# Optimization experiments

Measured on AMD Instinct MI355X. Metric: run time of the kernel, lower is better.

The kernel has to match this reference:

```python
import jax, jax.numpy as jnp
import numpy as np
import math

B, S, D, H = 4, 1024, 1024, 16
DK = D // H
NEG = -1e32


def _split_heads(x):
    # [B,S,D] -> [B,H,S,DK]
    return x.reshape(B, S, H, DK).transpose(0, 2, 1, 3)


def _merge_heads(x):
    # [B,H,S,DK] -> [B,S,D]
    return x.transpose(0, 2, 1, 3).reshape(B, S, D)


def _lin(x, w, b):
    # torch nn.Linear: y = x @ W^T + b, W is [out,in]
    return x @ w.T + b


def _decay_attn(scores, mask_f, gamma_val, pos):
    # scores: [B,H,S,S]; mask_f float {0,1}; gamma_val [1,H,1,1]; pos [S,S]
    def dist_fn(sc):
        p = jax.nn.softmax(jnp.where(mask_f == 0, NEG, sc), axis=-1) * mask_f
        cum = jnp.cumsum(p, axis=-1)
        tot = jnp.sum(p, axis=-1, keepdims=True)
        return jnp.sqrt(jnp.clip((tot - cum) * pos, 0.0))
    dist = jax.lax.stop_gradient(dist_fn(scores))  # torch.no_grad + detach
    eff = jnp.clip(jnp.exp(dist * gamma_val), 1e-5, 1e5)
    s = jnp.where(mask_f == 0, NEG, scores * eff)
    return jax.nn.softmax(s, axis=-1)


def _forward(mask, qmean, qcov, kmean, kcov, vmean, vcov,
             wq_m, bq_m, wq_c, bq_c, wk_m, bk_m, wk_c, bk_c,
             wv_m, bv_m, wv_c, bv_c, wo_m, bo_m, wo_c, bo_c, gammas):
    qm = _split_heads(_lin(qmean, wq_m, bq_m))
    qc = _split_heads(_lin(qcov, wq_c, bq_c))
    km = _split_heads(_lin(kmean, wk_m, bk_m))
    kc = _split_heads(_lin(kcov, wk_c, bk_c))
    vm = _split_heads(_lin(vmean, wv_m, bv_m))
    vc = _split_heads(_lin(vcov, wv_c, bv_c))

    scale = 1.0 / math.sqrt(DK)
    scores_mean = jnp.einsum('bhqd,bhkd->bhqk', qm, km) * scale
    scores_cov = jnp.einsum('bhqd,bhkd->bhqk', qc, kc) * scale

    mask_f = mask.astype(jnp.float32)
    idx = jnp.arange(S, dtype=jnp.float32)
    pos = jnp.abs(idx[None, :] - idx[:, None])  # |i-j| [S,S]
    gamma_val = -jax.nn.softplus(gammas)[None]  # [1,H,1,1]

    pm = _decay_attn(scores_mean, mask_f, gamma_val, pos)
    pc = _decay_attn(scores_cov, mask_f, gamma_val, pos)
    om = jnp.einsum('bhqk,bhkd->bhqd', pm, vm)
    oc = jnp.einsum('bhqk,bhkd->bhqd', pc, vc)

    out_mean = _lin(_merge_heads(om), wo_m, bo_m)
    out_cov = _lin(_merge_heads(oc), wo_c, bo_c)
    return out_mean, out_cov


def setup_inputs() -> dict:
    key = jax.random.key(0)
    ks = jax.random.split(key, 24)
    inp = {}
    tnames = ['query_mean', 'query_cov', 'key_mean', 'key_cov', 'values_mean', 'values_cov']
    for i, n in enumerate(tnames):
        inp[n] = jax.random.normal(ks[i], (B, S, D), jnp.float32)
    inp['mask'] = jnp.tril(jnp.ones((S, S), jnp.int32))[None, None]  # causal
    wnames = ['wq_m', 'wq_c', 'wk_m', 'wk_c', 'wv_m', 'wv_c', 'wo_m', 'wo_c']
    bound = math.sqrt(6.0 / (D + D))  # xavier_uniform
    for i, n in enumerate(wnames):
        inp[n] = jax.random.uniform(ks[6 + i], (D, D), jnp.float32, -bound, bound)
        inp['b' + n[1:]] = jnp.zeros((D,), jnp.float32)
    inp['gammas'] = jax.random.uniform(ks[20], (H, 1, 1), jnp.float32, -1.0, 1.0)
    return inp


def reference(query_mean, query_cov, key_mean, key_cov, values_mean, values_cov, mask,
              wq_m, bq_m, wq_c, bq_c, wk_m, bk_m, wk_c, bk_c,
              wv_m, bv_m, wv_c, bv_c, wo_m, bo_m, wo_c, bo_c, gammas):
    return _forward(mask, query_mean, query_cov, key_mean, key_cov, values_mean, values_cov,
                    wq_m, bq_m, wq_c, bq_c, wk_m, bk_m, wk_c, bk_c,
                    wv_m, bv_m, wv_c, bv_c, wo_m, bo_m, wo_c, bo_c, gammas)
```

## Files before the change

### kernel.cpp

```cpp
#include <hip/hip_runtime.h>
#include <math.h>

#define NTOK 4096
typedef unsigned int uint;

__device__ __forceinline__ int split_idx(int n, int d) {
  int b = n >> 10, s = n & 1023, h = d >> 6, dk = d & 63;
  return (((b << 4) + h) << 16) + (s << 6) + dk;
}

__device__ __forceinline__ ushort bf16_rne(float f) {
  uint u = __float_as_uint(f);
  return (ushort)((u + 0x7FFFu + ((u >> 16) & 1u)) >> 16);
}
__device__ __forceinline__ float bf16f(ushort h) {
  return __uint_as_float(((uint)h) << 16);
}

typedef __attribute__((ext_vector_type(8))) short bf16x8;
typedef __attribute__((ext_vector_type(4))) float f32x4;

__device__ __forceinline__ void gload16(const void* g, void* l) {
  __builtin_amdgcn_global_load_lds(
      (const __attribute__((address_space(1))) void*)g,
      (__attribute__((address_space(3))) void*)l, 16, 0, 0);
}

struct ConvP {
  const float4* s[14];
  ushort* hi[14];
  ushort* lo[14];
  int n4[14];
};
__global__ __launch_bounds__(256) void convert_split(ConvP C) {
  const int z = blockIdx.z;
  const int id = blockIdx.x * 256 + threadIdx.x;
  if (id >= C.n4[z]) return;
  const float4 x = C.s[z][id];
  const float xs[4] = {x.x, x.y, x.z, x.w};
  ushort hs[4], ls[4];
#pragma unroll
  for (int k = 0; k < 4; ++k) {
    hs[k] = bf16_rne(xs[k]);
    ls[k] = bf16_rne(xs[k] - bf16f(hs[k]));
  }
  ushort4 hv; hv.x = hs[0]; hv.y = hs[1]; hv.z = hs[2]; hv.w = hs[3];
  ushort4 lv; lv.x = ls[0]; lv.y = ls[1]; lv.z = ls[2]; lv.w = ls[3];
  *(ushort4*)&C.hi[z][id * 4] = hv;
  *(ushort4*)&C.lo[z][id * 4] = lv;
}

struct MG {
  const char* ah[6]; const char* al[6];
  const char* bh[6]; const char* bl[6];
  const float* bias[6]; float* y[6];
};

template<bool SPLIT_IN, bool SPLIT_OUT>
__global__ __launch_bounds__(256, 3) void gemm_mfma(MG P) {
  __shared__ ushort sAhi[4096], sAlo[4096], sBhi[4096], sBlo[4096];
  const int z = blockIdx.z;
  const char* __restrict__ Ah = P.ah[z];
  const char* __restrict__ Al = P.al[z];
  const char* __restrict__ Bh = P.bh[z];
  const char* __restrict__ Bl = P.bl[z];

  const int t = threadIdx.x, l = t & 63, w = t >> 6;
  const int wm = w >> 1, wn = w & 1;
  const int bn0 = blockIdx.x * 128, bm0 = blockIdx.y * 128;

  int offA[2], offB[2];
  {
    const int srow = w * 16 + (l >> 2), scd = l & 3;
#pragma unroll
    for (int q = 0; q < 2; ++q) {
      const int r = srow + q * 64;
      const int cc = scd ^ ((r >> 1) & 3);
      const int m = bm0 + r, n = bn0 + r;
      offA[q] = SPLIT_IN
                    ? ((((m >> 10) << 20) + ((m & 1023) << 6) + cc * 8) * 2)
                    : (m * 2048 + cc * 16);
      offB[q] = n * 2048 + cc * 16;
    }
  }
  int aoff[4], boff[4];
  {
    const int frow = l & 15, fc = l >> 4;
#pragma unroll
    for (int f = 0; f < 4; ++f) {
      const int ra = wm * 64 + f * 16 + frow;
      aoff[f] = ra * 64 + ((fc ^ ((ra >> 1) & 3)) * 16);
      const int rb = wn * 64 + f * 16 + frow;
      boff[f] = rb * 64 + ((fc ^ ((rb >> 1) & 3)) * 16);
    }
  }

  f32x4 acc[4][4];
#pragma unroll
  for (int i = 0; i < 4; ++i)
#pragma unroll
    for (int j = 0; j < 4; ++j) acc[i][j] = (f32x4){0.f, 0.f, 0.f, 0.f};

  for (int k0 = 0; k0 < 1024; k0 += 32) {
    __syncthreads();
    const int scA = SPLIT_IN ? ((((k0 >> 6) << 16) + (k0 & 63)) * 2) : (k0 * 2);
    const int scB = k0 * 2;
    gload16(Ah + offA[0] + scA, (char*)sAhi + w * 1024);
    gload16(Ah + offA[1] + scA, (char*)sAhi + 4096 + w * 1024);
    gload16(Al + offA[0] + scA, (char*)sAlo + w * 1024);
    gload16(Al + offA[1] + scA, (char*)sAlo + 4096 + w * 1024);
    gload16(Bh + offB[0] + scB, (char*)sBhi + w * 1024);
    gload16(Bh + offB[1] + scB, (char*)sBhi + 4096 + w * 1024);
    gload16(Bl + offB[0] + scB, (char*)sBlo + w * 1024);
    gload16(Bl + offB[1] + scB, (char*)sBlo + 4096 + w * 1024);
    __syncthreads();

    bf16x8 fah[4], fal[4], fbh[4], fbl[4];
#pragma unroll
    for (int f = 0; f < 4; ++f) {
      fah[f] = *(const bf16x8*)((const char*)sAhi + aoff[f]);
      fal[f] = *(const bf16x8*)((const char*)sAlo + aoff[f]);
      fbh[f] = *(const bf16x8*)((const char*)sBhi + boff[f]);
      fbl[f] = *(const bf16x8*)((const char*)sBlo + boff[f]);
    }
#pragma unroll
    for (int fi = 0; fi < 4; ++fi)
#pragma unroll
      for (int fj = 0; fj < 4; ++fj) {
        acc[fi][fj] = __builtin_amdgcn_mfma_f32_16x16x32_bf16(
            fah[fi], fbh[fj], acc[fi][fj], 0, 0, 0);
        acc[fi][fj] = __builtin_amdgcn_mfma_f32_16x16x32_bf16(
            fah[fi], fbl[fj], acc[fi][fj], 0, 0, 0);
        acc[fi][fj] = __builtin_amdgcn_mfma_f32_16x16x32_bf16(
            fal[fi], fbh[fj], acc[fi][fj], 0, 0, 0);
      }
  }

  const float* __restrict__ bias = P.bias[z];
  float* __restrict__ Y = P.y[z];
  float bv[4];
#pragma unroll
  for (int fj = 0; fj < 4; ++fj)
    bv[fj] = bias[bn0 + wn * 64 + fj * 16 + (l & 15)];
#pragma unroll
  for (int fi = 0; fi < 4; ++fi)
#pragma unroll
    for (int fj = 0; fj < 4; ++fj) {
      const int n = bn0 + wn * 64 + fj * 16 + (l & 15);
#pragma unroll
      for (int r = 0; r < 4; ++r) {
        const int m = bm0 + wm * 64 + fi * 16 + (l >> 4) * 4 + r;
        const float val = acc[fi][fj][r] + bv[fj];
        if constexpr (SPLIT_OUT) Y[split_idx(m, n)] = val;
        else Y[m * 1024 + n] = val;
      }
    }
}

struct GemmPtrs {
  const float* x[6]; const float* w[6]; const float* b[6]; float* y[6];
};
template<bool SPLIT_IN, bool SPLIT_OUT>
__global__ __launch_bounds__(256, 4) void gemm_kernel(GemmPtrs P) {
  const int z = blockIdx.z;
  const float* __restrict__ A = P.x[z];
  const float* __restrict__ W = P.w[z];
  const float* __restrict__ bias = P.b[z];
  float* __restrict__ Y = P.y[z];
  __shared__ float As[16][132];
  __shared__ float Bs[16][132];
  const int t = threadIdx.x;
  const int tx = t & 15, ty = t >> 4;
  const int bm0 = blockIdx.y * 128, bn0 = blockIdx.x * 128;
  float acc[8][8];
#pragma unroll
  for (int ii = 0; ii < 8; ++ii)
#pragma unroll
    for (int jj = 0; jj < 8; ++jj) acc[ii][jj] = 0.f;
  for (int k0 = 0; k0 < 1024; k0 += 16) {
    float4 av[2], bv[2];
#pragma unroll
    for (int q = 0; q < 2; ++q) {
      const int f = q * 256 + t, row = f >> 2, k4 = f & 3, gk = k0 + k4 * 4;
      if constexpr (SPLIT_IN) av[q] = *(const float4*)&A[split_idx(bm0 + row, gk)];
      else av[q] = *(const float4*)&A[(bm0 + row) * 1024 + gk];
      bv[q] = *(const float4*)&W[(bn0 + row) * 1024 + gk];
    }
    __syncthreads();
#pragma unroll
    for (int q = 0; q < 2; ++q) {
      const int f = q * 256 + t, row = f >> 2, k4 = f & 3;
      As[k4 * 4 + 0][row] = av[q].x; As[k4 * 4 + 1][row] = av[q].y;
      As[k4 * 4 + 2][row] = av[q].z; As[k4 * 4 + 3][row] = av[q].w;
      Bs[k4 * 4 + 0][row] = bv[q].x; Bs[k4 * 4 + 1][row] = bv[q].y;
      Bs[k4 * 4 + 2][row] = bv[q].z; Bs[k4 * 4 + 3][row] = bv[q].w;
    }
    __syncthreads();
#pragma unroll
    for (int k = 0; k < 16; ++k) {
      const float4 a0 = *(const float4*)&As[k][ty * 4];
      const float4 a1 = *(const float4*)&As[k][64 + ty * 4];
      const float4 b0 = *(const float4*)&Bs[k][tx * 4];
      const float4 b1 = *(const float4*)&Bs[k][64 + tx * 4];
      const float am[8] = {a0.x, a0.y, a0.z, a0.w, a1.x, a1.y, a1.z, a1.w};
      const float bn[8] = {b0.x, b0.y, b0.z, b0.w, b1.x, b1.y, b1.z, b1.w};
#pragma unroll
      for (int ii = 0; ii < 8; ++ii)
#pragma unroll
        for (int jj = 0; jj < 8; ++jj)
          acc[ii][jj] = fmaf(am[ii], bn[jj], acc[ii][jj]);
    }
  }
  const float4 bia0 = *(const float4*)&bias[bn0 + tx * 4];
  const float4 bia1 = *(const float4*)&bias[bn0 + 64 + tx * 4];
  const float bb[8] = {bia0.x, bia0.y, bia0.z, bia0.w,
                       bia1.x, bia1.y, bia1.z, bia1.w};
#pragma unroll
  for (int ii = 0; ii < 8; ++ii) {
    const int m = bm0 + ((ii < 4) ? (ty * 4 + ii) : (64 + ty * 4 + ii - 4));
    float4 r0, r1;
    r0.x = acc[ii][0] + bb[0]; r0.y = acc[ii][1] + bb[1];
    r0.z = acc[ii][2] + bb[2]; r0.w = acc[ii][3] + bb[3];
    r1.x = acc[ii][4] + bb[4]; r1.y = acc[ii][5] + bb[5];
    r1.z = acc[ii][6] + bb[6]; r1.w = acc[ii][7] + bb[7];
    if constexpr (SPLIT_OUT) {
      *(float4*)&Y[split_idx(m, bn0 + tx * 4)] = r0;
      *(float4*)&Y[split_idx(m, bn0 + 64 + tx * 4)] = r1;
    } else {
      *(float4*)&Y[m * 1024 + bn0 + tx * 4] = r0;
      *(float4*)&Y[m * 1024 + bn0 + 64 + tx * 4] = r1;
    }
  }
}

__device__ __forceinline__ float wmax64(float x) {
#pragma unroll
  for (int off = 32; off > 0; off >>= 1) x = fmaxf(x, __shfl_xor(x, off));
  return x;
}
__device__ __forceinline__ float wsum64(float x) {
#pragma unroll
  for (int off = 32; off > 0; off >>= 1) x += __shfl_xor(x, off);
  return x;
}

template<bool BF16OUT>
__global__ __launch_bounds__(256, 3) void decay_attn2(
    const float* __restrict__ qm, const float* __restrict__ km,
    const float* __restrict__ vm, const float* __restrict__ qc,
    const float* __restrict__ kc, const float* __restrict__ vc,
    float* __restrict__ om, float* __restrict__ oc,
    ushort* __restrict__ omh, ushort* __restrict__ oml,
    ushort* __restrict__ och, ushort* __restrict__ ocl,
    const float* __restrict__ gammas) {
  __shared__ float kvT[64][65];
  __shared__ float q_s[16][64];
  __shared__ float p_s[4][4][64];

  const int t = threadIdx.x, l = t & 63, w = t >> 6;
  const int bh = blockIdx.y, h = bh & 15;
  const int q0 = blockIdx.x * 16;
  const int path = blockIdx.z;
  const int base = bh << 16;
  const float* Q = (path ? qc : qm) + base;
  const float* K = (path ? kc : km) + base;
  const float* V = (path ? vc : vm) + base;
  const float g = -log1pf(__expf(gammas[h]));

  {
    const int row = t >> 4, d4 = t & 15;
    *(float4*)&q_s[row][d4 * 4] = *(const float4*)&Q[(q0 + row) * 64 + d4 * 4];
  }
  const int nchunks = (q0 >> 6) + 1;

  float v[4][16];
#pragma unroll
  for (int rr = 0; rr < 4; ++rr)
#pragma unroll
    for (int tt = 0; tt < 16; ++tt) v[rr][tt] = 0.f;

#pragma unroll 16
  for (int c = 0; c < 16; ++c) {
    if (c >= nchunks) break;
    if (c > 0) __syncthreads();
#pragma unroll
    for (int p = 0; p < 4; ++p) {
      const int f = p * 256 + t, j = f >> 4, d4 = f & 15;
      const float4 val = *(const float4*)&K[((c << 6) + j) * 64 + d4 * 4];
      kvT[d4 * 4 + 0][j] = val.x; kvT[d4 * 4 + 1][j] = val.y;
      kvT[d4 * 4 + 2][j] = val.z; kvT[d4 * 4 + 3][j] = val.w;
    }
    __syncthreads();
    float dots[4] = {0.f, 0.f, 0.f, 0.f};
#pragma unroll
    for (int d4 = 0; d4 < 16; ++d4) {
      const float k0v = kvT[d4 * 4 + 0][l], k1v = kvT[d4 * 4 + 1][l];
      const float k2v = kvT[d4 * 4 + 2][l], k3v = kvT[d4 * 4 + 3][l];
#pragma unroll
      for (int rr = 0; rr < 4; ++rr) {
        const float4 q4 = *(const float4*)&q_s[w + 4 * rr][d4 * 4];
        dots[rr] = fmaf(q4.x, k0v,
                   fmaf(q4.y, k1v, fmaf(q4.z, k2v, fmaf(q4.w, k3v, dots[rr]))));
      }
    }
#pragma unroll
    for (int rr = 0; rr < 4; ++rr) v[rr][c] = dots[rr] * 0.125f;
  }

#pragma unroll
  for (int rr = 0; rr < 4; ++rr) {
    const int i = q0 + w + 4 * rr;
    float m1 = -INFINITY;
#pragma unroll
    for (int g4 = 0; g4 < 4; ++g4) if (g4 * 4 < nchunks) {
#pragma unroll
      for (int u = 0; u < 4; ++u) {
        const int tt = g4 * 4 + u, j = tt * 64 + l;
        m1 = fmaxf(m1, (j <= i) ? v[rr][tt] : -INFINITY);
      }
    }
    m1 = wmax64(m1);

    float x[16], T[16];
    float zl = 0.f;
#pragma unroll
    for (int g4 = 0; g4 < 4; ++g4) if (g4 * 4 < nchunks) {
#pragma unroll
      for (int u = 0; u < 4; ++u) {
        const int tt = g4 * 4 + u, j = tt * 64 + l;
        x[tt] = (j <= i) ? __expf(v[rr][tt] - m1) : 0.f;
        zl += x[tt];
      }
    }
    const float rz1 = 1.f / wsum64(zl);
#pragma unroll
    for (int g4 = 0; g4 < 4; ++g4) if (g4 * 4 < nchunks) {
#pragma unroll
      for (int u = 0; u < 4; ++u) x[g4 * 4 + u] *= rz1;
    }
#pragma unroll
    for (int g4 = 0; g4 < 4; ++g4) if (g4 * 4 < nchunks) {
#pragma unroll
      for (int u = 0; u < 4; ++u) {
        const int tt = g4 * 4 + u;
#pragma unroll
        for (int off = 1; off < 64; off <<= 1) {
          const float nb = __shfl_up(x[tt], off);
          if (l >= off) x[tt] += nb;
        }
      }
    }
#pragma unroll
    for (int g4 = 0; g4 < 4; ++g4) if (g4 * 4 < nchunks) {
#pragma unroll
      for (int u = 0; u < 4; ++u) T[g4 * 4 + u] = __shfl(x[g4 * 4 + u], 63);
    }
    float tot = 0.f;
#pragma unroll
    for (int g4 = 0; g4 < 4; ++g4) if (g4 * 4 < nchunks) {
#pragma unroll
      for (int u = 0; u < 4; ++u) tot += T[g4 * 4 + u];
    }
    float run = 0.f, m2 = -INFINITY;
#pragma unroll
    for (int g4 = 0; g4 < 4; ++g4) if (g4 * 4 < nchunks) {
#pragma unroll
      for (int u = 0; u < 4; ++u) {
        const int tt = g4 * 4 + u, j = tt * 64 + l;
        const float cum = run + x[tt];
        run += T[tt];
        const float rem = fmaxf(tot - cum, 0.f);
        const float dist = sqrtf(fmaxf(rem * (float)(i - j), 0.f));
        float eff = __expf(dist * g);
        eff = fminf(fmaxf(eff, 1e-5f), 1e5f);
        const float s2 = (j <= i) ? v[rr][tt] * eff : -INFINITY;
        v[rr][tt] = s2;
        m2 = fmaxf(m2, s2);
      }
    }
    m2 = wmax64(m2);
    float z2 = 0.f;
#pragma unroll
    for (int g4 = 0; g4 < 4; ++g4) if (g4 * 4 < nchunks) {
#pragma unroll
      for (int u = 0; u < 4; ++u) {
        const int tt = g4 * 4 + u;
        const float e2 = __expf(v[rr][tt] - m2);
        v[rr][tt] = e2;
        z2 += e2;
      }
    }
    const float rz2 = 1.f / wsum64(z2);
#pragma unroll
    for (int g4 = 0; g4 < 4; ++g4) if (g4 * 4 < nchunks) {
#pragma unroll
      for (int u = 0; u < 4; ++u) v[rr][g4 * 4 + u] *= rz2;
    }
  }

  float acc[4] = {0.f, 0.f, 0.f, 0.f};
#pragma unroll 16
  for (int c = 0; c < 16; ++c) {
    if (c >= nchunks) break;
    __syncthreads();
#pragma unroll
    for (int p = 0; p < 4; ++p) {
      const int f = p * 256 + t, j = f >> 4, d4 = f & 15;
      const float4 val = *(const float4*)&V[((c << 6) + j) * 64 + d4 * 4];
      kvT[d4 * 4 + 0][j] = val.x; kvT[d4 * 4 + 1][j] = val.y;
      kvT[d4 * 4 + 2][j] = val.z; kvT[d4 * 4 + 3][j] = val.w;
    }
#pragma unroll
    for (int rr = 0; rr < 4; ++rr) p_s[w][rr][l] = v[rr][c];
    __syncthreads();
#pragma unroll
    for (int j4 = 0; j4 < 16; ++j4) {
      const float v0 = kvT[l][j4 * 4 + 0], v1 = kvT[l][j4 * 4 + 1];
      const float v2 = kvT[l][j4 * 4 + 2], v3 = kvT[l][j4 * 4 + 3];
#pragma unroll
      for (int rr = 0; rr < 4; ++rr) {
        const float4 p4 = *(const float4*)&p_s[w][rr][j4 * 4];
        acc[rr] = fmaf(p4.x, v0,
                  fmaf(p4.y, v1, fmaf(p4.z, v2, fmaf(p4.w, v3, acc[rr]))));
      }
    }
  }

#pragma unroll
  for (int rr = 0; rr < 4; ++rr) {
    const int i = q0 + w + 4 * rr;
    const int idx = base + i * 64 + l;
    if constexpr (BF16OUT) {
      const ushort hb = bf16_rne(acc[rr]);
      const ushort lb = bf16_rne(acc[rr] - bf16f(hb));
      (path ? och : omh)[idx] = hb;
      (path ? ocl : oml)[idx] = lb;
    } else {
      (path ? oc : om)[idx] = acc[rr];
    }
  }
}

extern "C" void kernel_launch(void* const* d_in, const int* in_sizes, int n_in,
                              void* d_out, int out_size, void* d_ws,
                              size_t ws_size, hipStream_t stream) {
  (void)in_sizes; (void)n_in; (void)out_size;

  const float* X[6];
  for (int i = 0; i < 6; ++i) X[i] = (const float*)d_in[i];
  const float* Wt[8]; const float* Bs[8];
  for (int i = 0; i < 8; ++i) {
    Wt[i] = (const float*)d_in[7 + 2 * i];
    Bs[i] = (const float*)d_in[8 + 2 * i];
  }
  const float* gam = (const float*)d_in[23];
  float* out_mean = (float*)d_out;
  float* out_cov = out_mean + (size_t)NTOK * 1024;

  const size_t MB = 1024ull * 1024ull;
  const size_t NEED = 224ull * MB;
  char* ws = (char*)d_ws;

  if (ws_size >= NEED) {
    ushort* Xhi = (ushort*)(ws + 0);
    ushort* Xlo = (ushort*)(ws + 48 * MB);
    ushort* Whi = (ushort*)(ws + 96 * MB);
    ushort* Wlo = (ushort*)(ws + 112 * MB);
    float* QKV = (float*)(ws + 128 * MB);
    ushort* OMh = (ushort*)(ws + 0 * MB);
    ushort* OMl = (ushort*)(ws + 8 * MB);
    ushort* OCh = (ushort*)(ws + 16 * MB);
    ushort* OCl = (ushort*)(ws + 24 * MB);

    const size_t XE = 4194304, WE = 1048576, QE = 4194304;

    ConvP C = {};
    for (int i = 0; i < 6; ++i) {
      C.s[i] = (const float4*)X[i];
      C.hi[i] = Xhi + (size_t)i * XE;
      C.lo[i] = Xlo + (size_t)i * XE;
      C.n4[i] = (int)(XE / 4);
    }
    for (int i = 0; i < 8; ++i) {
      C.s[6 + i] = (const float4*)Wt[i];
      C.hi[6 + i] = Whi + (size_t)i * WE;
      C.lo[6 + i] = Wlo + (size_t)i * WE;
      C.n4[6 + i] = (int)(WE / 4);
    }
    convert_split<<<dim3(4096, 1, 14), 256, 0, stream>>>(C);

    MG Pin = {};
    for (int z = 0; z < 6; ++z) {
      Pin.ah[z] = (const char*)(Xhi + (size_t)z * XE);
      Pin.al[z] = (const char*)(Xlo + (size_t)z * XE);
      Pin.bh[z] = (const char*)(Whi + (size_t)z * WE);
      Pin.bl[z] = (const char*)(Wlo + (size_t)z * WE);
      Pin.bias[z] = Bs[z];
      Pin.y[z] = QKV + (size_t)z * QE;
    }
    gemm_mfma<false, true><<<dim3(8, 32, 6), 256, 0, stream>>>(Pin);

    float* qm = QKV + 0 * QE; float* qc = QKV + 1 * QE;
    float* km = QKV + 2 * QE; float* kc = QKV + 3 * QE;
    float* vm = QKV + 4 * QE; float* vc = QKV + 5 * QE;
    decay_attn2<true><<<dim3(64, 64, 2), 256, 0, stream>>>(
        qm, km, vm, qc, kc, vc, nullptr, nullptr, OMh, OMl, OCh, OCl, gam);

    MG Pout = {};
    Pout.ah[0] = (const char*)OMh; Pout.al[0] = (const char*)OMl;
    Pout.bh[0] = (const char*)(Whi + 6 * WE);
    Pout.bl[0] = (const char*)(Wlo + 6 * WE);
    Pout.bias[0] = Bs[6]; Pout.y[0] = out_mean;
    Pout.ah[1] = (const char*)OCh; Pout.al[1] = (const char*)OCl;
    Pout.bh[1] = (const char*)(Whi + 7 * WE);
    Pout.bl[1] = (const char*)(Wlo + 7 * WE);
    Pout.bias[1] = Bs[7]; Pout.y[1] = out_cov;
    gemm_mfma<true, false><<<dim3(8, 32, 2), 256, 0, stream>>>(Pout);
  } else {
    float* qkv = (float*)ws;
    float* om = (float*)(ws + 96 * MB);
    float* ocv = (float*)(ws + 112 * MB);
    const size_t QE = 4194304;

    GemmPtrs Pin = {};
    for (int z = 0; z < 6; ++z) {
      Pin.x[z] = X[z]; Pin.w[z] = Wt[z]; Pin.b[z] = Bs[z];
      Pin.y[z] = qkv + (size_t)z * QE;
    }
    gemm_kernel<false, true><<<dim3(8, 32, 6), 256, 0, stream>>>(Pin);

    decay_attn2<false><<<dim3(64, 64, 2), 256, 0, stream>>>(
        qkv + 0 * QE, qkv + 2 * QE, qkv + 4 * QE, qkv + 1 * QE, qkv + 3 * QE,
        qkv + 5 * QE, om, ocv, nullptr, nullptr, nullptr, nullptr, gam);

    GemmPtrs Pout = {};
    Pout.x[0] = om; Pout.w[0] = Wt[6]; Pout.b[0] = Bs[6]; Pout.y[0] = out_mean;
    Pout.x[1] = ocv; Pout.w[1] = Wt[7]; Pout.b[1] = Bs[7]; Pout.y[1] = out_cov;
    gemm_kernel<true, false><<<dim3(8, 32, 2), 256, 0, stream>>>(Pout);
  }
}
```

Baseline: 1.365 ms.

## Rewrite decay attention with 64-row query tiles and double-buffered async K/V loads

The attention kernel now handles 64 query rows per 512-thread block instead of 16 rows per 256-thread block, so each K/V chunk is loaded once for four times as many rows. K and V chunks are loaded with async global-to-LDS copies into a double-buffered, XOR-swizzled shared buffer, replacing the transposing register stores. The next chunk is prefetched while the current one is computed. Dot products use packed float2 FMAs, and the probability normalisation is folded into the decay exponent. The changes target the redundant global traffic and synchronisation per chunk, at the cost of more registers per thread (v[8][16]), larger LDS use, and fewer blocks with a coarser causal load imbalance.

```diff
diff --git a/kernel.cpp b/kernel.cpp
--- a/kernel.cpp
+++ b/kernel.cpp
@@ -245,7 +245,7 @@
 }
 
 template<bool BF16OUT>
-__global__ __launch_bounds__(256, 3) void decay_attn2(
+__global__ __launch_bounds__(512, 4) void decay_attn3(
     const float* __restrict__ qm, const float* __restrict__ km,
     const float* __restrict__ vm, const float* __restrict__ qc,
     const float* __restrict__ kc, const float* __restrict__ vc,
@@ -253,13 +253,14 @@
     ushort* __restrict__ omh, ushort* __restrict__ oml,
     ushort* __restrict__ och, ushort* __restrict__ ocl,
     const float* __restrict__ gammas) {
-  __shared__ float kvT[64][65];
-  __shared__ float q_s[16][64];
-  __shared__ float p_s[4][4][64];
+  __shared__ __align__(16) char kvraw[2][16384];
+  __shared__ float q_s[64][64];
+  __shared__ float p_s[8][8][64];
 
   const int t = threadIdx.x, l = t & 63, w = t >> 6;
   const int bh = blockIdx.y, h = bh & 15;
-  const int q0 = blockIdx.x * 16;
+  const int q0 = blockIdx.x * 64;
+  const int nchunks = blockIdx.x + 1;
   const int path = blockIdx.z;
   const int base = bh << 16;
   const float* Q = (path ? qc : qm) + base;
@@ -267,176 +268,189 @@
   const float* V = (path ? vc : vm) + base;
   const float g = -log1pf(__expf(gammas[h]));
 
-  {
-    const int row = t >> 4, d4 = t & 15;
-    *(float4*)&q_s[row][d4 * 4] = *(const float4*)&Q[(q0 + row) * 64 + d4 * 4];
-  }
-  const int nchunks = (q0 >> 6) + 1;
-
-  float v[4][16];
-#pragma unroll
-  for (int rr = 0; rr < 4; ++rr)
-#pragma unroll
-    for (int tt = 0; tt < 16; ++tt) v[rr][tt] = 0.f;
-
-#pragma unroll 16
+#pragma unroll
+  for (int qq = 0; qq < 2; ++qq) {
+    const int f = qq * 512 + t, row = f >> 4, c4 = f & 15;
+    *(float4*)&q_s[row][c4 * 4] = *(const float4*)&Q[(q0 + row) * 64 + c4 * 4];
+  }
+#pragma unroll
+  for (int qq = 0; qq < 2; ++qq) {
+    const int f = qq * 512 + t, j = f >> 4, cc = f & 15;
+    gload16((const char*)K + (j << 8) + ((cc ^ (j & 7)) << 4),
+            &kvraw[0][0] + qq * 8192 + w * 1024);
+  }
+  __syncthreads();
+
+  float v[8][16];
+
+#pragma unroll
   for (int c = 0; c < 16; ++c) {
-    if (c >= nchunks) break;
-    if (c > 0) __syncthreads();
-#pragma unroll
-    for (int p = 0; p < 4; ++p) {
-      const int f = p * 256 + t, j = f >> 4, d4 = f & 15;
-      const float4 val = *(const float4*)&K[((c << 6) + j) * 64 + d4 * 4];
-      kvT[d4 * 4 + 0][j] = val.x; kvT[d4 * 4 + 1][j] = val.y;
-      kvT[d4 * 4 + 2][j] = val.z; kvT[d4 * 4 + 3][j] = val.w;
-    }
-    __syncthreads();
-    float dots[4] = {0.f, 0.f, 0.f, 0.f};
-#pragma unroll
-    for (int d4 = 0; d4 < 16; ++d4) {
-      const float k0v = kvT[d4 * 4 + 0][l], k1v = kvT[d4 * 4 + 1][l];
-      const float k2v = kvT[d4 * 4 + 2][l], k3v = kvT[d4 * 4 + 3][l];
-#pragma unroll
-      for (int rr = 0; rr < 4; ++rr) {
-        const float4 q4 = *(const float4*)&q_s[w + 4 * rr][d4 * 4];
-        dots[rr] = fmaf(q4.x, k0v,
-                   fmaf(q4.y, k1v, fmaf(q4.z, k2v, fmaf(q4.w, k3v, dots[rr]))));
-      }
-    }
-#pragma unroll
-    for (int rr = 0; rr < 4; ++rr) v[rr][c] = dots[rr] * 0.125f;
-  }
-
-#pragma unroll
-  for (int rr = 0; rr < 4; ++rr) {
-    const int i = q0 + w + 4 * rr;
+    if (c < nchunks) {
+      if (c + 1 < nchunks) {
+        const char* Ksrc = (const char*)K + (((c + 1) << 6) << 8);
+#pragma unroll
+        for (int qq = 0; qq < 2; ++qq) {
+          const int f = qq * 512 + t, j = f >> 4, cc = f & 15;
+          gload16(Ksrc + (j << 8) + ((cc ^ (j & 7)) << 4),
+                  &kvraw[(c + 1) & 1][0] + qq * 8192 + w * 1024);
+        }
+      }
+      const char* kb = &kvraw[c & 1][0];
+      float2 d2[8];
+#pragma unroll
+      for (int rr = 0; rr < 8; ++rr) d2[rr] = make_float2(0.f, 0.f);
+#pragma unroll
+      for (int g4 = 0; g4 < 4; ++g4) {
+        float4 kr[4];
+#pragma unroll
+        for (int u = 0; u < 4; ++u) {
+          const int c4 = g4 * 4 + u;
+          kr[u] = *(const float4*)(kb + l * 256 + ((c4 ^ (l & 7)) << 4));
+        }
+#pragma unroll
+        for (int rr = 0; rr < 8; ++rr) {
+#pragma unroll
+          for (int u = 0; u < 4; ++u) {
+            const float4 q4 = *(const float4*)&q_s[w * 8 + rr][(g4 * 4 + u) * 4];
+            d2[rr] += make_float2(q4.x, q4.y) * make_float2(kr[u].x, kr[u].y)
+                    + make_float2(q4.z, q4.w) * make_float2(kr[u].z, kr[u].w);
+          }
+        }
+      }
+#pragma unroll
+      for (int rr = 0; rr < 8; ++rr)
+        v[rr][c] = (d2[rr].x + d2[rr].y) * 0.125f;
+      __syncthreads();
+    }
+  }
+
+#pragma unroll
+  for (int qq = 0; qq < 2; ++qq) {
+    const int f = qq * 512 + t, j = f >> 4, cc = f & 15;
+    gload16((const char*)V + (j << 8) + ((cc ^ (j & 7)) << 4),
+            &kvraw[0][0] + qq * 8192 + w * 1024);
+  }
+
+#pragma unroll
+  for (int rr = 0; rr < 8; ++rr) {
+    const int i = q0 + w * 8 + rr;
     float m1 = -INFINITY;
 #pragma unroll
-    for (int g4 = 0; g4 < 4; ++g4) if (g4 * 4 < nchunks) {
-#pragma unroll
-      for (int u = 0; u < 4; ++u) {
-        const int tt = g4 * 4 + u, j = tt * 64 + l;
+    for (int tt = 0; tt < 16; ++tt)
+      if (tt < nchunks) {
+        const int j = tt * 64 + l;
         m1 = fmaxf(m1, (j <= i) ? v[rr][tt] : -INFINITY);
       }
-    }
     m1 = wmax64(m1);
 
     float x[16], T[16];
     float zl = 0.f;
 #pragma unroll
-    for (int g4 = 0; g4 < 4; ++g4) if (g4 * 4 < nchunks) {
-#pragma unroll
-      for (int u = 0; u < 4; ++u) {
-        const int tt = g4 * 4 + u, j = tt * 64 + l;
+    for (int tt = 0; tt < 16; ++tt)
+      if (tt < nchunks) {
+        const int j = tt * 64 + l;
         x[tt] = (j <= i) ? __expf(v[rr][tt] - m1) : 0.f;
         zl += x[tt];
       }
-    }
     const float rz1 = 1.f / wsum64(zl);
-#pragma unroll
-    for (int g4 = 0; g4 < 4; ++g4) if (g4 * 4 < nchunks) {
-#pragma unroll
-      for (int u = 0; u < 4; ++u) x[g4 * 4 + u] *= rz1;
-    }
-#pragma unroll
-    for (int g4 = 0; g4 < 4; ++g4) if (g4 * 4 < nchunks) {
-#pragma unroll
-      for (int u = 0; u < 4; ++u) {
-        const int tt = g4 * 4 + u;
+
+#pragma unroll
+    for (int tt = 0; tt < 16; ++tt)
+      if (tt < nchunks) {
 #pragma unroll
         for (int off = 1; off < 64; off <<= 1) {
           const float nb = __shfl_up(x[tt], off);
           if (l >= off) x[tt] += nb;
         }
-      }
-    }
-#pragma unroll
-    for (int g4 = 0; g4 < 4; ++g4) if (g4 * 4 < nchunks) {
-#pragma unroll
-      for (int u = 0; u < 4; ++u) T[g4 * 4 + u] = __shfl(x[g4 * 4 + u], 63);
-    }
+        T[tt] = __shfl(x[tt], 63);
+      }
     float tot = 0.f;
 #pragma unroll
-    for (int g4 = 0; g4 < 4; ++g4) if (g4 * 4 < nchunks) {
-#pragma unroll
-      for (int u = 0; u < 4; ++u) tot += T[g4 * 4 + u];
-    }
+    for (int tt = 0; tt < 16; ++tt)
+      if (tt < nchunks) tot += T[tt];
+
+    const float gs = g * sqrtf(rz1);
     float run = 0.f, m2 = -INFINITY;
 #pragma unroll
-    for (int g4 = 0; g4 < 4; ++g4) if (g4 * 4 < nchunks) {
-#pragma unroll
-      for (int u = 0; u < 4; ++u) {
-        const int tt = g4 * 4 + u, j = tt * 64 + l;
+    for (int tt = 0; tt < 16; ++tt)
+      if (tt < nchunks) {
+        const int j = tt * 64 + l;
         const float cum = run + x[tt];
         run += T[tt];
-        const float rem = fmaxf(tot - cum, 0.f);
-        const float dist = sqrtf(fmaxf(rem * (float)(i - j), 0.f));
-        float eff = __expf(dist * g);
+        const float dist = sqrtf(fmaxf((tot - cum) * (float)(i - j), 0.f));
+        float eff = __expf(gs * dist);
         eff = fminf(fmaxf(eff, 1e-5f), 1e5f);
         const float s2 = (j <= i) ? v[rr][tt] * eff : -INFINITY;
         v[rr][tt] = s2;
         m2 = fmaxf(m2, s2);
       }
-    }
     m2 = wmax64(m2);
+
     float z2 = 0.f;
 #pragma unroll
-    for (int g4 = 0; g4 < 4; ++g4) if (g4 * 4 < nchunks) {
-#pragma unroll
-      for (int u = 0; u < 4; ++u) {
-        const int tt = g4 * 4 + u;
+    for (int tt = 0; tt < 16; ++tt)
+      if (tt < nchunks) {
         const float e2 = __expf(v[rr][tt] - m2);
         v[rr][tt] = e2;
         z2 += e2;
       }
-    }
     const float rz2 = 1.f / wsum64(z2);
 #pragma unroll
-    for (int g4 = 0; g4 < 4; ++g4) if (g4 * 4 < nchunks) {
-#pragma unroll
-      for (int u = 0; u < 4; ++u) v[rr][g4 * 4 + u] *= rz2;
-    }
-  }
-
-  float acc[4] = {0.f, 0.f, 0.f, 0.f};
-#pragma unroll 16
+    for (int tt = 0; tt < 16; ++tt)
+      if (tt < nchunks) v[rr][tt] *= rz2;
+  }
+  __syncthreads();
+
+  float2 acc2[8];
+#pragma unroll
+  for (int rr = 0; rr < 8; ++rr) acc2[rr] = make_float2(0.f, 0.f);
+#pragma unroll
   for (int c = 0; c < 16; ++c) {
-    if (c >= nchunks) break;
-    __syncthreads();
-#pragma unroll
-    for (int p = 0; p < 4; ++p) {
-      const int f = p * 256 + t, j = f >> 4, d4 = f & 15;
-      const float4 val = *(const float4*)&V[((c << 6) + j) * 64 + d4 * 4];
-      kvT[d4 * 4 + 0][j] = val.x; kvT[d4 * 4 + 1][j] = val.y;
-      kvT[d4 * 4 + 2][j] = val.z; kvT[d4 * 4 + 3][j] = val.w;
-    }
-#pragma unroll
-    for (int rr = 0; rr < 4; ++rr) p_s[w][rr][l] = v[rr][c];
-    __syncthreads();
-#pragma unroll
-    for (int j4 = 0; j4 < 16; ++j4) {
-      const float v0 = kvT[l][j4 * 4 + 0], v1 = kvT[l][j4 * 4 + 1];
-      const float v2 = kvT[l][j4 * 4 + 2], v3 = kvT[l][j4 * 4 + 3];
-#pragma unroll
-      for (int rr = 0; rr < 4; ++rr) {
-        const float4 p4 = *(const float4*)&p_s[w][rr][j4 * 4];
-        acc[rr] = fmaf(p4.x, v0,
-                  fmaf(p4.y, v1, fmaf(p4.z, v2, fmaf(p4.w, v3, acc[rr]))));
-      }
-    }
-  }
-
-#pragma unroll
-  for (int rr = 0; rr < 4; ++rr) {
-    const int i = q0 + w + 4 * rr;
+    if (c < nchunks) {
+      if (c + 1 < nchunks) {
+        const char* Vsrc = (const char*)V + (((c + 1) << 6) << 8);
+#pragma unroll
+        for (int qq = 0; qq < 2; ++qq) {
+          const int f = qq * 512 + t, j = f >> 4, cc = f & 15;
+          gload16(Vsrc + (j << 8) + ((cc ^ (j & 7)) << 4),
+                  &kvraw[(c + 1) & 1][0] + qq * 8192 + w * 1024);
+        }
+      }
+      const char* vb = &kvraw[c & 1][0];
+#pragma unroll
+      for (int rr = 0; rr < 8; ++rr) p_s[w][rr][l] = v[rr][c];
+#pragma unroll
+      for (int j4 = 0; j4 < 16; ++j4) {
+        float vj[4];
+#pragma unroll
+        for (int u = 0; u < 4; ++u) {
+          const int j = j4 * 4 + u;
+          vj[u] = *(const float*)(vb + (j << 8) +
+                                  ((((l >> 2) ^ (j & 7))) << 4) + ((l & 3) << 2));
+        }
+#pragma unroll
+        for (int rr = 0; rr < 8; ++rr) {
+          const float4 p4 = *(const float4*)&p_s[w][rr][j4 * 4];
+          acc2[rr] += make_float2(p4.x, p4.y) * make_float2(vj[0], vj[1])
+                    + make_float2(p4.z, p4.w) * make_float2(vj[2], vj[3]);
+        }
+      }
+      __syncthreads();
+    }
+  }
+
+#pragma unroll
+  for (int rr = 0; rr < 8; ++rr) {
+    const int i = q0 + w * 8 + rr;
     const int idx = base + i * 64 + l;
+    const float a = acc2[rr].x + acc2[rr].y;
     if constexpr (BF16OUT) {
-      const ushort hb = bf16_rne(acc[rr]);
-      const ushort lb = bf16_rne(acc[rr] - bf16f(hb));
+      const ushort hb = bf16_rne(a);
+      const ushort lb = bf16_rne(a - bf16f(hb));
       (path ? och : omh)[idx] = hb;
       (path ? ocl : oml)[idx] = lb;
     } else {
-      (path ? oc : om)[idx] = acc[rr];
+      (path ? oc : om)[idx] = a;
     }
   }
 }
@@ -503,7 +517,7 @@
     float* qm = QKV + 0 * QE; float* qc = QKV + 1 * QE;
     float* km = QKV + 2 * QE; float* kc = QKV + 3 * QE;
     float* vm = QKV + 4 * QE; float* vc = QKV + 5 * QE;
-    decay_attn2<true><<<dim3(64, 64, 2), 256, 0, stream>>>(
+    decay_attn3<true><<<dim3(16, 64, 2), 512, 0, stream>>>(
         qm, km, vm, qc, kc, vc, nullptr, nullptr, OMh, OMl, OCh, OCl, gam);
 
     MG Pout = {};
@@ -529,7 +543,7 @@
     }
     gemm_kernel<false, true><<<dim3(8, 32, 6), 256, 0, stream>>>(Pin);
 
-    decay_attn2<false><<<dim3(64, 64, 2), 256, 0, stream>>>(
+    decay_attn3<false><<<dim3(16, 64, 2), 512, 0, stream>>>(
         qkv + 0 * QE, qkv + 2 * QE, qkv + 4 * QE, qkv + 1 * QE, qkv + 3 * QE,
         qkv + 5 * QE, om, ocv, nullptr, nullptr, nullptr, nullptr, gam);
 
```

After: 1.833 ms. +34.2%, slower.
